# Performance work log

Hardware: AMD Instinct MI355X
Metric: run time of the kernel (lower is better)

## Reference

```python
import jax, jax.numpy as jnp
import numpy as np

B, T, I, H, L = 64, 512, 512, 512, 2

def _xavier(key, shape):
    fan_in, fan_out = shape
    limit = float(np.sqrt(6.0 / (fan_in + fan_out)))
    return jax.random.uniform(key, shape, jnp.float32, -limit, limit)

def setup_inputs() -> dict:
    key = jax.random.key(0)
    ks = jax.random.split(key, 16)
    x = jax.random.normal(ks[0], (B, T, I), jnp.float32)
    h = jax.random.normal(ks[1], (L, B, H), jnp.float32)
    c = jax.random.normal(ks[2], (L, B, H), jnp.float32)
    # Gate order: i, f, g, o (concatenated along output dim -> [*, 4H])
    W_x0 = jnp.concatenate([_xavier(ks[3 + j], (I, H)) for j in range(4)], axis=1)
    W_h0 = jnp.concatenate([_xavier(ks[7 + j], (H, H)) for j in range(4)], axis=1)
    W_x1 = jnp.concatenate([_xavier(ks[11], (H, H)), _xavier(ks[12], (H, H)),
                            _xavier(ks[13], (H, H)), _xavier(ks[14], (H, H))], axis=1)
    W_h1 = jnp.concatenate([jax.random.split(ks[15], 4)[j] is None or _xavier(jax.random.split(ks[15], 4)[j], (H, H)) for j in range(4)], axis=1)
    # 8 scalar biases per layer: (b_ii, b_hi, b_if, b_hf, b_ig, b_hg, b_io, b_ho); zero-init as in torch
    b0 = jnp.zeros((8,), jnp.float32)
    b1 = jnp.zeros((8,), jnp.float32)
    return {"x": x, "h": h, "c": c, "W_x0": W_x0, "W_h0": W_h0, "b0": b0,
            "W_x1": W_x1, "W_h1": W_h1, "b1": b1}

def _lstm_layer(xs, h0, c0, Wx, Wh, b):
    # xs: [B, T, D]; Wx: [D, 4H]; Wh: [H, 4H]; b: [8] scalars
    bg = b[0::2] + b[1::2]  # combined per-gate scalar biases [4]: i, f, g, o
    x_proj = jnp.einsum('btd,dk->btk', xs, Wx)  # precompute input GEMM: [B, T, 4H]

    def step(carry, xp_t):
        h, c = carry
        z = xp_t + h @ Wh  # [B, 4H]
        zi, zf, zg, zo = jnp.split(z, 4, axis=1)
        i = jax.nn.sigmoid(zi + bg[0])
        f = jax.nn.sigmoid(zf + bg[1])
        g = jnp.tanh(zg + bg[2])
        o = jax.nn.sigmoid(zo + bg[3])
        c_new = f * c + i * g
        h_new = o * jnp.tanh(c_new)
        return (h_new, c_new), h_new

    (hT, cT), ys = jax.lax.scan(step, (h0, c0), jnp.swapaxes(x_proj, 0, 1))
    return jnp.swapaxes(ys, 0, 1), hT, cT  # output [B, T, H]

def reference(x, h, c, W_x0, W_h0, b0, W_x1, W_h1, b1):
    out0, h0T, c0T = _lstm_layer(x, h[0], c[0], W_x0, W_h0, b0)
    out1, h1T, c1T = _lstm_layer(out0, h[1], c[1], W_x1, W_h1, b1)
    new_h = jnp.stack([h0T, h1T])  # [L, B, H]
    new_c = jnp.stack([c0T, c1T])
    return out1, new_h, new_c
```

## Files before the change

### kernel.cpp

```cpp
#include <hip/hip_runtime.h>
#include <hip/hip_bf16.h>

#define B_   64
#define T_   512
#define I_   512
#define H_   512
#define NBLK 128
#define NTHR 256

typedef short bf16x8 __attribute__((ext_vector_type(8)));
typedef float f32x4  __attribute__((ext_vector_type(4)));
typedef unsigned long long u64;
typedef unsigned short u16;

#define MFMA(a, b, c) __builtin_amdgcn_mfma_f32_16x16x32_bf16((a), (b), (c), 0, 0, 0)

__device__ __forceinline__ u16 f2b(float f) {
    __hip_bfloat16 h = __float2bfloat16(f);
    return __builtin_bit_cast(u16, h);
}

__device__ __forceinline__ u64 coh_ld64(const void* p) {
    return __hip_atomic_load((const u64*)p, __ATOMIC_RELAXED, __HIP_MEMORY_SCOPE_AGENT);
}
__device__ __forceinline__ void coh_st64(void* p, u64 v) {
    __hip_atomic_store((u64*)p, v, __ATOMIC_RELAXED, __HIP_MEMORY_SCOPE_AGENT);
}

__device__ __forceinline__ bool flag_ge(const int* f, int idx, int tgt) {
    return __hip_atomic_load(f + idx, __ATOMIC_RELAXED, __HIP_MEMORY_SCOPE_AGENT) >= tgt;
}

__global__ void k_init(const float* __restrict__ x, const float* __restrict__ h,
                       u16* __restrict__ xb, u16* __restrict__ h0ring, u16* __restrict__ h1ring,
                       int* __restrict__ flags0, int* __restrict__ flags1) {
    long i = (long)blockIdx.x * 256 + threadIdx.x;
    if (i < 2097152) {
        const float* p = x + i * 8;
        float4 a = *(const float4*)p;
        float4 b = *(const float4*)(p + 4);
        union { u16 s[8]; bf16x8 v; } u;
        u.s[0]=f2b(a.x); u.s[1]=f2b(a.y); u.s[2]=f2b(a.z); u.s[3]=f2b(a.w);
        u.s[4]=f2b(b.x); u.s[5]=f2b(b.y); u.s[6]=f2b(b.z); u.s[7]=f2b(b.w);
        *(bf16x8*)(xb + i * 8) = u.v;
    } else if (i < 2097152 + 8192) {
        long j = i - 2097152;
        const float* p = h + j * 8;
        #pragma unroll
        for (int jj = 0; jj < 8; ++jj) {
            long idx = j * 8 + jj;
            u16 v = f2b(p[jj]);
            if (idx < 32768) h0ring[7 * 32768 + idx] = v;
            else             h1ring[7 * 32768 + (idx - 32768)] = v;
        }
    } else if (i < 2097152 + 8192 + 512) {
        int j = (int)(i - (2097152 + 8192));
        if (j < 256) flags0[j] = 0; else flags1[j - 256] = 0;
    }
}

__global__ __launch_bounds__(NTHR, 1) void k_lstm(
    const u16* __restrict__ xb,
    const float* __restrict__ Wx0, const float* __restrict__ Wh0, const float* __restrict__ b0,
    const float* __restrict__ Wx1, const float* __restrict__ Wh1, const float* __restrict__ b1,
    const float* __restrict__ c_in,
    u16* __restrict__ h0ring, u16* __restrict__ h1ring,
    int* __restrict__ flags0, int* __restrict__ flags1,
    float* __restrict__ cs,
    float* __restrict__ out)
{
    const int tid  = threadIdx.x;
    const int bid  = blockIdx.x;
    const int lay  = bid >> 6;
    const int g    = (bid >> 4) & 3;
    const int u    = bid & 15;
    const int wave = tid >> 6;
    const int lane = tid & 63;
    const int n    = lane & 15;
    const int quad = lane >> 4;
    const int R0   = g * 16;
    const int U0   = u * 32;

    __shared__ __align__(16) u16   hstage[2][8192];
    __shared__ __align__(16) u16   sc_all[16 * 36];
    __shared__ __align__(16) float sc_h [4][16][8];

    const float* Wx = lay ? Wx1 : Wx0;
    const float* Wh = lay ? Wh1 : Wh0;
    const float* bb = lay ? b1  : b0;
    const float bi = bb[0] + bb[1];
    const float bf = bb[2] + bb[3];
    const float bg = bb[4] + bb[5];
    const float bo = bb[6] + bb[7];

    bf16x8 breg[2][32];
    #pragma unroll
    for (int ct = 0; ct < 2; ++ct) {
        const int gate = ct * 2 + (n >> 3);
        const int gcol = gate * 512 + U0 + wave * 8 + (n & 7);
        #pragma unroll
        for (int f = 0; f < 32; ++f) {
            const int kbase = f * 32 + quad * 8;
            bf16x8 w;
            #pragma unroll
            for (int j = 0; j < 8; ++j) {
                const int k = kbase + j;
                const float v = (k < 512) ? Wx[(size_t)k * 2048 + gcol]
                                          : Wh[(size_t)(k - 512) * 2048 + gcol];
                w[j] = (short)f2b(v);
            }
            breg[ct][f] = w;
        }
    }

    int* myflag = (lay ? flags1 : flags0) + g * 16 + u;
    const int fidx = g * 16 + n;
    (void)cs;

    float creg[4];
    if (n < 8) {
        #pragma unroll
        for (int r = 0; r < 4; ++r)
            creg[r] = c_in[(size_t)lay * 32768
                           + (size_t)(R0 + quad * 4 + r) * 512 + U0 + wave * 8 + n];
    }

    for (int t = 0; t < 512; ++t) {
        f32x4 acc0 = {0.f, 0.f, 0.f, 0.f};
        f32x4 acc1 = {0.f, 0.f, 0.f, 0.f};

        if (lay == 0) {
            const u16* px = xb + ((size_t)(R0 + n) * T_ + t) * I_;
            bf16x8 xa[16];
            #pragma unroll
            for (int f = 0; f < 16; ++f) xa[f] = *(const bf16x8*)(px + f * 32 + quad * 8);
            #pragma unroll
            for (int f = 0; f < 16; ++f) {
                acc0 = MFMA(xa[f], breg[0][f], acc0);
                acc1 = MFMA(xa[f], breg[1][f], acc1);
            }
            const bool bp = (t & 3) == 0;
            for (;;) {
                bool ok = flag_ge(flags0, fidx, t);
                if (bp) ok = ok && flag_ge(flags1, fidx, t - 4);
                if (__all(ok)) break;
                __builtin_amdgcn_s_sleep(1);
            }
            asm volatile("" ::: "memory");
            const u16* base = h0ring + (size_t)((t - 1) & 7) * 32768;
            u64 v[8];
            #pragma unroll
            for (int i = 0; i < 8; ++i) {
                const int s = i * 256 + tid;
                const int r = s >> 7, m = s & 127;
                v[i] = coh_ld64(base + (size_t)(R0 + r) * 512 + m * 4);
            }
            #pragma unroll
            for (int i = 0; i < 8; ++i) {
                const int s = i * 256 + tid;
                const int r = s >> 7, m = s & 127;
                const int uu = m >> 1, sub = m & 1;
                *(u64*)&hstage[0][r * 512 + (((uu ^ (r & 7)) << 3) | (sub << 2))] = v[i];
            }
            __syncthreads();
            #pragma unroll
            for (int f = 0; f < 16; ++f) {
                bf16x8 ha = *(const bf16x8*)
                    &hstage[0][n * 512 + (((f * 4 + quad) ^ (n & 7)) << 3)];
                acc0 = MFMA(ha, breg[0][16 + f], acc0);
                acc1 = MFMA(ha, breg[1][16 + f], acc1);
            }
        } else {
            for (;;) {
                bool ok = flag_ge(flags1, fidx, t) && flag_ge(flags0, fidx, t + 1);
                if (__all(ok)) break;
                __builtin_amdgcn_s_sleep(1);
            }
            asm volatile("" ::: "memory");
            const u16* base0 = h0ring + (size_t)(t & 7) * 32768;
            const u16* base1 = h1ring + (size_t)((t - 1) & 7) * 32768;
            u64 v0[8], v1[8];
            #pragma unroll
            for (int i = 0; i < 8; ++i) {
                const int s = i * 256 + tid;
                const int r = s >> 7, m = s & 127;
                v0[i] = coh_ld64(base0 + (size_t)(R0 + r) * 512 + m * 4);
                v1[i] = coh_ld64(base1 + (size_t)(R0 + r) * 512 + m * 4);
            }
            #pragma unroll
            for (int i = 0; i < 8; ++i) {
                const int s = i * 256 + tid;
                const int r = s >> 7, m = s & 127;
                const int uu = m >> 1, sub = m & 1;
                const int off = r * 512 + (((uu ^ (r & 7)) << 3) | (sub << 2));
                *(u64*)&hstage[0][off] = v0[i];
                *(u64*)&hstage[1][off] = v1[i];
            }
            __syncthreads();
            #pragma unroll
            for (int f = 0; f < 16; ++f) {
                const int off = n * 512 + (((f * 4 + quad) ^ (n & 7)) << 3);
                bf16x8 ha = *(const bf16x8*)&hstage[0][off];
                acc0 = MFMA(ha, breg[0][f], acc0);
                acc1 = MFMA(ha, breg[1][f], acc1);
                bf16x8 hb = *(const bf16x8*)&hstage[1][off];
                acc0 = MFMA(hb, breg[0][16 + f], acc0);
                acc1 = MFMA(hb, breg[1][16 + f], acc1);
            }
        }

        f32x4 x0, x1;
        #pragma unroll
        for (int r = 0; r < 4; ++r) {
            x0[r] = __shfl_xor(acc0[r], 8);
            x1[r] = __shfl_xor(acc1[r], 8);
        }
        if (n < 8) {
            #pragma unroll
            for (int r = 0; r < 4; ++r) {
                const int row = quad * 4 + r;
                const float zi = acc0[r] + bi;
                const float zf = x0[r]   + bf;
                const float zg = acc1[r] + bg;
                const float zo = x1[r]   + bo;
                const float ig = 1.f / (1.f + __expf(-zi));
                const float fg = 1.f / (1.f + __expf(-zf));
                const float gg = tanhf(zg);
                const float og = 1.f / (1.f + __expf(-zo));
                const float cn = fg * creg[r] + ig * gg;
                const float hn = og * tanhf(cn);
                creg[r] = cn;
                sc_all[row * 36 + wave * 8 + n] = f2b(hn);
                sc_h [wave][row][n] = hn;
            }
        }
        __syncthreads();

        if (wave == 0) {
            u16* ring = (lay ? h1ring : h0ring) + (size_t)(t & 7) * 32768;
            #pragma unroll
            for (int k = 0; k < 2; ++k) {
                const int j   = k * 64 + lane;
                const int row = j >> 3, s8 = j & 7;
                u64 vv = *(const u64*)&sc_all[row * 36 + s8 * 4];
                coh_st64(ring + (size_t)(R0 + row) * 512 + U0 + s8 * 4, vv);
            }
            asm volatile("s_waitcnt vmcnt(0)" ::: "memory");
            if (lane == 0)
                __hip_atomic_store(myflag, t + 1, __ATOMIC_RELAXED, __HIP_MEMORY_SCOPE_AGENT);
        }

        if (lay && lane < 16) {
            const float* s = &sc_h[wave][lane][0];
            f32x4 a  = *(const f32x4*)s;
            f32x4 b2 = *(const f32x4*)(s + 4);
            float* po = out + ((size_t)(R0 + lane) * T_ + t) * H_ + U0 + wave * 8;
            *(f32x4*)po       = a;
            *(f32x4*)(po + 4) = b2;
        }
        if (t == 511 && n < 8) {
            const size_t o1 = (size_t)B_ * T_ * H_;
            #pragma unroll
            for (int r = 0; r < 4; ++r) {
                const int grow = R0 + quad * 4 + r;
                out[o1 +         (size_t)lay * 32768 + (size_t)grow * 512 + U0 + wave * 8 + n]
                    = sc_h[wave][quad * 4 + r][n];
                out[o1 + 65536 + (size_t)lay * 32768 + (size_t)grow * 512 + U0 + wave * 8 + n]
                    = creg[r];
            }
        }
    }
}

extern "C" void kernel_launch(void* const* d_in, const int* in_sizes, int n_in,
                              void* d_out, int out_size, void* d_ws, size_t ws_size,
                              hipStream_t stream) {
    const float* x   = (const float*)d_in[0];
    const float* h   = (const float*)d_in[1];
    const float* c   = (const float*)d_in[2];
    const float* Wx0 = (const float*)d_in[3];
    const float* Wh0 = (const float*)d_in[4];
    const float* b0  = (const float*)d_in[5];
    const float* Wx1 = (const float*)d_in[6];
    const float* Wh1 = (const float*)d_in[7];
    const float* b1  = (const float*)d_in[8];
    float* out = (float*)d_out;

    u16* xb     = (u16*)d_ws;
    u16* h0ring = xb + 16777216;
    u16* h1ring = h0ring + 262144;
    int* flags0 = (int*)(h1ring + 262144);
    int* flags1 = flags0 + 256;
    float* cs   = (float*)(flags1 + 256);

    k_init<<<8226, 256, 0, stream>>>(x, h, xb, h0ring, h1ring, flags0, flags1);
    k_lstm<<<NBLK, NTHR, 0, stream>>>(xb, Wx0, Wh0, b0, Wx1, Wh1, b1, c,
                                      h0ring, h1ring, flags0, flags1, cs, out);
}
```

Baseline: 3.138 ms.

## Co-locate batch groups on one XCD and sync via L2-coherent sc0 accesses

Launches 256 blocks and keeps only half of them, then reads the hardware XCC id so each batch group's 32 blocks can check whether they share one XCD. If they do and an sc0 probe round-trip succeeds, the recurrent h ring and flags use sc0 global loads and stores that stay coherent within that XCD's L2, and h is read straight from global instead of being staged through LDS. Otherwise the kernel falls back to the original agent-scope atomic path. This aims to cut the per-step cross-XCD synchronisation latency, at the cost of depending on how the hardware schedules blocks onto XCDs, extra startup handshakes, and spin loops with no sleep.

Result: faster. 2.938 ms (-6.4%).

```diff
diff --git a/kernel.cpp b/kernel.cpp
--- a/kernel.cpp
+++ b/kernel.cpp
@@ -5,7 +5,6 @@
 #define T_   512
 #define I_   512
 #define H_   512
-#define NBLK 128
 #define NTHR 256
 
 typedef short bf16x8 __attribute__((ext_vector_type(8)));
@@ -26,14 +25,76 @@
 __device__ __forceinline__ void coh_st64(void* p, u64 v) {
     __hip_atomic_store((u64*)p, v, __ATOMIC_RELAXED, __HIP_MEMORY_SCOPE_AGENT);
 }
-
 __device__ __forceinline__ bool flag_ge(const int* f, int idx, int tgt) {
     return __hip_atomic_load(f + idx, __ATOMIC_RELAXED, __HIP_MEMORY_SCOPE_AGENT) >= tgt;
 }
 
-__global__ void k_init(const float* __restrict__ x, const float* __restrict__ h,
-                       u16* __restrict__ xb, u16* __restrict__ h0ring, u16* __restrict__ h1ring,
-                       int* __restrict__ flags0, int* __restrict__ flags1) {
+__device__ __forceinline__ int sc0_ld_i32(const int* p) {
+    int v;
+    asm volatile("global_load_dword %0, %1, off sc0\n\ts_waitcnt vmcnt(0)"
+                 : "=&v"(v) : "v"(p) : "memory");
+    return v;
+}
+__device__ __forceinline__ void sc0_st_i32(int* p, int v) {
+    asm volatile("global_store_dword %0, %1, off sc0" :: "v"(p), "v"(v) : "memory");
+}
+
+#define GLD16(O, A)                                                         \
+  asm volatile(                                                             \
+    "global_load_dwordx4 %0, %16, off sc0\n\t"                              \
+    "global_load_dwordx4 %1, %16, off offset:64 sc0\n\t"                    \
+    "global_load_dwordx4 %2, %16, off offset:128 sc0\n\t"                   \
+    "global_load_dwordx4 %3, %16, off offset:192 sc0\n\t"                   \
+    "global_load_dwordx4 %4, %16, off offset:256 sc0\n\t"                   \
+    "global_load_dwordx4 %5, %16, off offset:320 sc0\n\t"                   \
+    "global_load_dwordx4 %6, %16, off offset:384 sc0\n\t"                   \
+    "global_load_dwordx4 %7, %16, off offset:448 sc0\n\t"                   \
+    "global_load_dwordx4 %8, %16, off offset:512 sc0\n\t"                   \
+    "global_load_dwordx4 %9, %16, off offset:576 sc0\n\t"                   \
+    "global_load_dwordx4 %10, %16, off offset:640 sc0\n\t"                  \
+    "global_load_dwordx4 %11, %16, off offset:704 sc0\n\t"                  \
+    "global_load_dwordx4 %12, %16, off offset:768 sc0\n\t"                  \
+    "global_load_dwordx4 %13, %16, off offset:832 sc0\n\t"                  \
+    "global_load_dwordx4 %14, %16, off offset:896 sc0\n\t"                  \
+    "global_load_dwordx4 %15, %16, off offset:960 sc0\n\t"                  \
+    "s_waitcnt vmcnt(0)"                                                    \
+    : "=&v"(O[0]), "=&v"(O[1]), "=&v"(O[2]), "=&v"(O[3]),                   \
+      "=&v"(O[4]), "=&v"(O[5]), "=&v"(O[6]), "=&v"(O[7]),                   \
+      "=&v"(O[8]), "=&v"(O[9]), "=&v"(O[10]), "=&v"(O[11]),                 \
+      "=&v"(O[12]), "=&v"(O[13]), "=&v"(O[14]), "=&v"(O[15])                \
+    : "v"(A) : "memory")
+
+__device__ __forceinline__ void pub_local(u16* ring, int* fp, int fval,
+                                          const u16* sca, int lane, int U0) {
+    const int r0 = lane >> 3, s0 = lane & 7;
+    const int r1 = 8 + r0;
+    u64 q0 = *(const u64*)(sca + r0 * 36 + s0 * 4);
+    u64 q1 = *(const u64*)(sca + r1 * 36 + s0 * 4);
+    u16* d0 = ring + r0 * 512 + U0 + s0 * 4;
+    u16* d1 = ring + r1 * 512 + U0 + s0 * 4;
+    asm volatile(
+        "global_store_dwordx2 %0, %2, off sc0\n\t"
+        "global_store_dwordx2 %1, %3, off sc0\n\t"
+        "s_waitcnt vmcnt(0)"
+        :: "v"(d0), "v"(d1), "v"(q0), "v"(q1) : "memory");
+    if (lane == 0) sc0_st_i32(fp, fval);
+}
+
+__device__ __forceinline__ void pub_agent(u16* ring, int* fp, int fval,
+                                          const u16* sca, int lane, int R0, int U0) {
+    const int r0 = lane >> 3, s0 = lane & 7;
+    const int r1 = 8 + r0;
+    u64 q0 = *(const u64*)(sca + r0 * 36 + s0 * 4);
+    u64 q1 = *(const u64*)(sca + r1 * 36 + s0 * 4);
+    coh_st64(ring + (size_t)(R0 + r0) * 512 + U0 + s0 * 4, q0);
+    coh_st64(ring + (size_t)(R0 + r1) * 512 + U0 + s0 * 4, q1);
+    asm volatile("s_waitcnt vmcnt(0)" ::: "memory");
+    if (lane == 0)
+        __hip_atomic_store(fp, fval, __ATOMIC_RELAXED, __HIP_MEMORY_SCOPE_AGENT);
+}
+
+__global__ void k_init(const float* __restrict__ x, u16* __restrict__ xb,
+                       int* __restrict__ fl) {
     long i = (long)blockIdx.x * 256 + threadIdx.x;
     if (i < 2097152) {
         const float* p = x + i * 8;
@@ -43,19 +104,8 @@
         u.s[0]=f2b(a.x); u.s[1]=f2b(a.y); u.s[2]=f2b(a.z); u.s[3]=f2b(a.w);
         u.s[4]=f2b(b.x); u.s[5]=f2b(b.y); u.s[6]=f2b(b.z); u.s[7]=f2b(b.w);
         *(bf16x8*)(xb + i * 8) = u.v;
-    } else if (i < 2097152 + 8192) {
-        long j = i - 2097152;
-        const float* p = h + j * 8;
-        #pragma unroll
-        for (int jj = 0; jj < 8; ++jj) {
-            long idx = j * 8 + jj;
-            u16 v = f2b(p[jj]);
-            if (idx < 32768) h0ring[7 * 32768 + idx] = v;
-            else             h1ring[7 * 32768 + (idx - 32768)] = v;
-        }
-    } else if (i < 2097152 + 8192 + 512) {
-        int j = (int)(i - (2097152 + 8192));
-        if (j < 256) flags0[j] = 0; else flags1[j - 256] = 0;
+    } else if (i < 2097152 + 1024) {
+        fl[i - 2097152] = -1;
     }
 }
 
@@ -63,17 +113,21 @@
     const u16* __restrict__ xb,
     const float* __restrict__ Wx0, const float* __restrict__ Wh0, const float* __restrict__ b0,
     const float* __restrict__ Wx1, const float* __restrict__ Wh1, const float* __restrict__ b1,
-    const float* __restrict__ c_in,
-    u16* __restrict__ h0ring, u16* __restrict__ h1ring,
-    int* __restrict__ flags0, int* __restrict__ flags1,
-    float* __restrict__ cs,
+    const float* __restrict__ c_in, const float* __restrict__ h_in,
+    u16* __restrict__ h0ag, u16* __restrict__ h1ag,
+    u16* __restrict__ h0loc, u16* __restrict__ h1loc,
+    int* __restrict__ f0ag, int* __restrict__ f1ag,
+    int* __restrict__ f0loc, int* __restrict__ f1loc,
+    int* __restrict__ xcc_tab, int* __restrict__ probe, int* __restrict__ verd,
     float* __restrict__ out)
 {
+    const int bid = blockIdx.x;
+    if ((bid & 7) >= 4) return;
+    const int g   = bid & 7;
+    const int jj  = bid >> 3;
+    const int lay = jj >> 4;
+    const int u   = jj & 15;
     const int tid  = threadIdx.x;
-    const int bid  = blockIdx.x;
-    const int lay  = bid >> 6;
-    const int g    = (bid >> 4) & 3;
-    const int u    = bid & 15;
     const int wave = tid >> 6;
     const int lane = tid & 63;
     const int n    = lane & 15;
@@ -84,6 +138,13 @@
     __shared__ __align__(16) u16   hstage[2][8192];
     __shared__ __align__(16) u16   sc_all[16 * 36];
     __shared__ __align__(16) float sc_h [4][16][8];
+    __shared__ int s_local;
+    __shared__ int s_ver;
+
+    int myxcc;
+    asm volatile("s_getreg_b32 %0, hwreg(HW_REG_XCC_ID)" : "=s"(myxcc));
+    if (tid == 0)
+        __hip_atomic_store(xcc_tab + bid, myxcc, __ATOMIC_RELAXED, __HIP_MEMORY_SCOPE_AGENT);
 
     const float* Wx = lay ? Wx1 : Wx0;
     const float* Wh = lay ? Wh1 : Wh0;
@@ -113,10 +174,6 @@
         }
     }
 
-    int* myflag = (lay ? flags1 : flags0) + g * 16 + u;
-    const int fidx = g * 16 + n;
-    (void)cs;
-
     float creg[4];
     if (n < 8) {
         #pragma unroll
@@ -125,10 +182,220 @@
                            + (size_t)(R0 + quad * 4 + r) * 512 + U0 + wave * 8 + n];
     }
 
+    if (wave == 0) {
+        const int member = (lane & 31) * 8 + g;
+        int v;
+        for (;;) {
+            v = __hip_atomic_load(xcc_tab + member, __ATOMIC_RELAXED, __HIP_MEMORY_SCOPE_AGENT);
+            if (__all(v != -1)) break;
+            __builtin_amdgcn_s_sleep(8);
+        }
+        const int v0 = __shfl(v, 0);
+        if (lane == 0) s_local = __all(v == v0) ? 1 : 0;
+    }
+    __syncthreads();
+
+    int myver = 0;
+    if (s_local) {
+        if (tid == 0) sc0_st_i32(probe + bid, 0x5a5a0000 | bid);
+        if (wave == 0) {
+            const int member = (lane & 31) * 8 + g;
+            const int want = 0x5a5a0000 | member;
+            int ok = 0;
+            for (int it = 0; it < 4000 && !ok; ++it)
+                ok = __all(sc0_ld_i32(probe + member) == want) ? 1 : 0;
+            if (lane == 0) s_ver = ok;
+        }
+        __syncthreads();
+        myver = s_ver;
+    }
+
+    if (tid == 0)
+        __hip_atomic_store(verd + bid, myver, __ATOMIC_RELAXED, __HIP_MEMORY_SCOPE_AGENT);
+    if (wave == 0) {
+        const int member = (lane & 31) * 8 + g;
+        int v;
+        for (;;) {
+            v = __hip_atomic_load(verd + member, __ATOMIC_RELAXED, __HIP_MEMORY_SCOPE_AGENT);
+            if (__all(v != -1)) break;
+            __builtin_amdgcn_s_sleep(8);
+        }
+        if (lane == 0) s_local = __all(v == 1) ? 1 : 0;
+    }
+    __syncthreads();
+    const bool loc = (s_local != 0);
+
+    if (n < 8) {
+        #pragma unroll
+        for (int r = 0; r < 4; ++r) {
+            const int row = quad * 4 + r;
+            const float hv = h_in[(size_t)lay * 32768
+                                  + (size_t)(R0 + row) * 512 + U0 + wave * 8 + n];
+            sc_all[row * 36 + wave * 8 + n] = f2b(hv);
+        }
+    }
+    __syncthreads();
+    if (loc) {
+        if (wave == 3)
+            pub_local((lay ? h1loc : h0loc) + (size_t)g * 65536 + 7 * 8192,
+                      (lay ? f1loc : f0loc) + g * 16 + u, 0, sc_all, lane, U0);
+    } else {
+        if (wave == 0)
+            pub_agent((lay ? h1ag : h0ag) + (size_t)7 * 32768,
+                      (lay ? f1ag : f0ag) + g * 16 + u, 0, sc_all, lane, R0, U0);
+    }
+
+    const int fidx = g * 16 + n;
+
+    if (loc) {
+        int* pp0 = f0loc + g * 16 + n;
+        int* pp1 = f1loc + g * 16 + n;
+        if (lay == 0) {
+            for (int t = 0; t < 512; ++t) {
+                f32x4 acc0 = {0.f,0.f,0.f,0.f}, acc1 = {0.f,0.f,0.f,0.f};
+                const u16* px = xb + ((size_t)(R0 + n) * T_ + t) * I_;
+                bf16x8 xa[16];
+                #pragma unroll
+                for (int f = 0; f < 16; ++f) xa[f] = *(const bf16x8*)(px + f * 32 + quad * 8);
+                #pragma unroll
+                for (int f = 0; f < 16; ++f) {
+                    acc0 = MFMA(xa[f], breg[0][f], acc0);
+                    acc1 = MFMA(xa[f], breg[1][f], acc1);
+                }
+                if ((t & 3) == 0) {
+                    for (;;) {
+                        int a_ = sc0_ld_i32(pp0);
+                        int b_ = sc0_ld_i32(pp1);
+                        if (__all(a_ >= t && b_ >= t - 4)) break;
+                    }
+                } else {
+                    while (!__all(sc0_ld_i32(pp0) >= t)) {}
+                }
+                const u16* ha = h0loc + (size_t)g * 65536
+                                + (size_t)((t - 1) & 7) * 8192 + n * 512 + quad * 8;
+                bf16x8 hf[16];
+                GLD16(hf, ha);
+                #pragma unroll
+                for (int f = 0; f < 16; ++f) {
+                    acc0 = MFMA(hf[f], breg[0][16 + f], acc0);
+                    acc1 = MFMA(hf[f], breg[1][16 + f], acc1);
+                }
+                f32x4 x0, x1;
+                #pragma unroll
+                for (int r = 0; r < 4; ++r) {
+                    x0[r] = __shfl_xor(acc0[r], 8);
+                    x1[r] = __shfl_xor(acc1[r], 8);
+                }
+                if (n < 8) {
+                    #pragma unroll
+                    for (int r = 0; r < 4; ++r) {
+                        const int row = quad * 4 + r;
+                        const float zi = acc0[r] + bi, zf = x0[r] + bf;
+                        const float zg = acc1[r] + bg, zo = x1[r] + bo;
+                        const float ig = 1.f / (1.f + __expf(-zi));
+                        const float fg = 1.f / (1.f + __expf(-zf));
+                        const float gg = tanhf(zg);
+                        const float og = 1.f / (1.f + __expf(-zo));
+                        const float cn = fg * creg[r] + ig * gg;
+                        const float hn = og * tanhf(cn);
+                        creg[r] = cn;
+                        sc_all[row * 36 + wave * 8 + n] = f2b(hn);
+                        sc_h[wave][row][n] = hn;
+                    }
+                }
+                __syncthreads();
+                if (wave == (t & 3))
+                    pub_local(h0loc + (size_t)g * 65536 + (size_t)(t & 7) * 8192,
+                              f0loc + g * 16 + u, t + 1, sc_all, lane, U0);
+                if (t == 511 && n < 8) {
+                    const size_t o1 = (size_t)B_ * T_ * H_;
+                    #pragma unroll
+                    for (int r = 0; r < 4; ++r) {
+                        const int grow = R0 + quad * 4 + r;
+                        out[o1 + (size_t)grow * 512 + U0 + wave * 8 + n]
+                            = sc_h[wave][quad * 4 + r][n];
+                        out[o1 + 65536 + (size_t)grow * 512 + U0 + wave * 8 + n] = creg[r];
+                    }
+                }
+            }
+        } else {
+            for (int t = 0; t < 512; ++t) {
+                for (;;) {
+                    int a_ = sc0_ld_i32(pp1);
+                    int b_ = sc0_ld_i32(pp0);
+                    if (__all(a_ >= t && b_ >= t + 1)) break;
+                }
+                const u16* a0p = h0loc + (size_t)g * 65536
+                                 + (size_t)(t & 7) * 8192 + n * 512 + quad * 8;
+                const u16* a1p = h1loc + (size_t)g * 65536
+                                 + (size_t)((t - 1) & 7) * 8192 + n * 512 + quad * 8;
+                f32x4 acc0 = {0.f,0.f,0.f,0.f}, acc1 = {0.f,0.f,0.f,0.f};
+                bf16x8 hf[16];
+                GLD16(hf, a0p);
+                #pragma unroll
+                for (int f = 0; f < 16; ++f) {
+                    acc0 = MFMA(hf[f], breg[0][f], acc0);
+                    acc1 = MFMA(hf[f], breg[1][f], acc1);
+                }
+                GLD16(hf, a1p);
+                #pragma unroll
+                for (int f = 0; f < 16; ++f) {
+                    acc0 = MFMA(hf[f], breg[0][16 + f], acc0);
+                    acc1 = MFMA(hf[f], breg[1][16 + f], acc1);
+                }
+                f32x4 x0, x1;
+                #pragma unroll
+                for (int r = 0; r < 4; ++r) {
+                    x0[r] = __shfl_xor(acc0[r], 8);
+                    x1[r] = __shfl_xor(acc1[r], 8);
+                }
+                if (n < 8) {
+                    #pragma unroll
+                    for (int r = 0; r < 4; ++r) {
+                        const int row = quad * 4 + r;
+                        const float zi = acc0[r] + bi, zf = x0[r] + bf;
+                        const float zg = acc1[r] + bg, zo = x1[r] + bo;
+                        const float ig = 1.f / (1.f + __expf(-zi));
+                        const float fg = 1.f / (1.f + __expf(-zf));
+                        const float gg = tanhf(zg);
+                        const float og = 1.f / (1.f + __expf(-zo));
+                        const float cn = fg * creg[r] + ig * gg;
+                        const float hn = og * tanhf(cn);
+                        creg[r] = cn;
+                        sc_all[row * 36 + wave * 8 + n] = f2b(hn);
+                        sc_h[wave][row][n] = hn;
+                    }
+                }
+                __syncthreads();
+                if (wave == (t & 3))
+                    pub_local(h1loc + (size_t)g * 65536 + (size_t)(t & 7) * 8192,
+                              f1loc + g * 16 + u, t + 1, sc_all, lane, U0);
+                if (lane < 16) {
+                    const float* s = &sc_h[wave][lane][0];
+                    f32x4 a  = *(const f32x4*)s;
+                    f32x4 b2 = *(const f32x4*)(s + 4);
+                    float* po = out + ((size_t)(R0 + lane) * T_ + t) * H_ + U0 + wave * 8;
+                    *(f32x4*)po       = a;
+                    *(f32x4*)(po + 4) = b2;
+                }
+                if (t == 511 && n < 8) {
+                    const size_t o1 = (size_t)B_ * T_ * H_;
+                    #pragma unroll
+                    for (int r = 0; r < 4; ++r) {
+                        const int grow = R0 + quad * 4 + r;
+                        out[o1 + 32768 + (size_t)grow * 512 + U0 + wave * 8 + n]
+                            = sc_h[wave][quad * 4 + r][n];
+                        out[o1 + 65536 + 32768 + (size_t)grow * 512 + U0 + wave * 8 + n]
+                            = creg[r];
+                    }
+                }
+            }
+        }
+        return;
+    }
+
     for (int t = 0; t < 512; ++t) {
-        f32x4 acc0 = {0.f, 0.f, 0.f, 0.f};
-        f32x4 acc1 = {0.f, 0.f, 0.f, 0.f};
-
+        f32x4 acc0 = {0.f,0.f,0.f,0.f}, acc1 = {0.f,0.f,0.f,0.f};
         if (lay == 0) {
             const u16* px = xb + ((size_t)(R0 + n) * T_ + t) * I_;
             bf16x8 xa[16];
@@ -141,13 +408,13 @@
             }
             const bool bp = (t & 3) == 0;
             for (;;) {
-                bool ok = flag_ge(flags0, fidx, t);
-                if (bp) ok = ok && flag_ge(flags1, fidx, t - 4);
+                bool ok = flag_ge(f0ag, fidx, t);
+                if (bp) ok = ok && flag_ge(f1ag, fidx, t - 4);
                 if (__all(ok)) break;
                 __builtin_amdgcn_s_sleep(1);
             }
             asm volatile("" ::: "memory");
-            const u16* base = h0ring + (size_t)((t - 1) & 7) * 32768;
+            const u16* base = h0ag + (size_t)((t - 1) & 7) * 32768;
             u64 v[8];
             #pragma unroll
             for (int i = 0; i < 8; ++i) {
@@ -172,13 +439,13 @@
             }
         } else {
             for (;;) {
-                bool ok = flag_ge(flags1, fidx, t) && flag_ge(flags0, fidx, t + 1);
+                bool ok = flag_ge(f1ag, fidx, t) && flag_ge(f0ag, fidx, t + 1);
                 if (__all(ok)) break;
                 __builtin_amdgcn_s_sleep(1);
             }
             asm volatile("" ::: "memory");
-            const u16* base0 = h0ring + (size_t)(t & 7) * 32768;
-            const u16* base1 = h1ring + (size_t)((t - 1) & 7) * 32768;
+            const u16* base0 = h0ag + (size_t)(t & 7) * 32768;
+            const u16* base1 = h1ag + (size_t)((t - 1) & 7) * 32768;
             u64 v0[8], v1[8];
             #pragma unroll
             for (int i = 0; i < 8; ++i) {
@@ -208,7 +475,6 @@
                 acc1 = MFMA(hb, breg[1][16 + f], acc1);
             }
         }
-
         f32x4 x0, x1;
         #pragma unroll
         for (int r = 0; r < 4; ++r) {
@@ -219,10 +485,8 @@
             #pragma unroll
             for (int r = 0; r < 4; ++r) {
                 const int row = quad * 4 + r;
-                const float zi = acc0[r] + bi;
-                const float zf = x0[r]   + bf;
-                const float zg = acc1[r] + bg;
-                const float zo = x1[r]   + bo;
+                const float zi = acc0[r] + bi, zf = x0[r] + bf;
+                const float zg = acc1[r] + bg, zo = x1[r] + bo;
                 const float ig = 1.f / (1.f + __expf(-zi));
                 const float fg = 1.f / (1.f + __expf(-zf));
                 const float gg = tanhf(zg);
@@ -231,25 +495,13 @@
                 const float hn = og * tanhf(cn);
                 creg[r] = cn;
                 sc_all[row * 36 + wave * 8 + n] = f2b(hn);
-                sc_h [wave][row][n] = hn;
+                sc_h[wave][row][n] = hn;
             }
         }
         __syncthreads();
-
-        if (wave == 0) {
-            u16* ring = (lay ? h1ring : h0ring) + (size_t)(t & 7) * 32768;
-            #pragma unroll
-            for (int k = 0; k < 2; ++k) {
-                const int j   = k * 64 + lane;
-                const int row = j >> 3, s8 = j & 7;
-                u64 vv = *(const u64*)&sc_all[row * 36 + s8 * 4];
-                coh_st64(ring + (size_t)(R0 + row) * 512 + U0 + s8 * 4, vv);
-            }
-            asm volatile("s_waitcnt vmcnt(0)" ::: "memory");
-            if (lane == 0)
-                __hip_atomic_store(myflag, t + 1, __ATOMIC_RELAXED, __HIP_MEMORY_SCOPE_AGENT);
-        }
-
+        if (wave == 0)
+            pub_agent((lay ? h1ag : h0ag) + (size_t)(t & 7) * 32768,
+                      (lay ? f1ag : f0ag) + g * 16 + u, t + 1, sc_all, lane, R0, U0);
         if (lay && lane < 16) {
             const float* s = &sc_h[wave][lane][0];
             f32x4 a  = *(const f32x4*)s;
@@ -263,7 +515,7 @@
             #pragma unroll
             for (int r = 0; r < 4; ++r) {
                 const int grow = R0 + quad * 4 + r;
-                out[o1 +         (size_t)lay * 32768 + (size_t)grow * 512 + U0 + wave * 8 + n]
+                out[o1 + (size_t)lay * 32768 + (size_t)grow * 512 + U0 + wave * 8 + n]
                     = sc_h[wave][quad * 4 + r][n];
                 out[o1 + 65536 + (size_t)lay * 32768 + (size_t)grow * 512 + U0 + wave * 8 + n]
                     = creg[r];
@@ -287,13 +539,20 @@
     float* out = (float*)d_out;
 
     u16* xb     = (u16*)d_ws;
-    u16* h0ring = xb + 16777216;
-    u16* h1ring = h0ring + 262144;
-    int* flags0 = (int*)(h1ring + 262144);
-    int* flags1 = flags0 + 256;
-    float* cs   = (float*)(flags1 + 256);
-
-    k_init<<<8226, 256, 0, stream>>>(x, h, xb, h0ring, h1ring, flags0, flags1);
-    k_lstm<<<NBLK, NTHR, 0, stream>>>(xb, Wx0, Wh0, b0, Wx1, Wh1, b1, c,
-                                      h0ring, h1ring, flags0, flags1, cs, out);
-}
+    u16* h0ag   = xb + 16777216;
+    u16* h1ag   = h0ag + 262144;
+    u16* h0loc  = h1ag + 262144;
+    u16* h1loc  = h0loc + 262144;
+    int* f0ag   = (int*)(h1loc + 262144);
+    int* f1ag   = f0ag + 64;
+    int* f0loc  = f1ag + 64;
+    int* f1loc  = f0loc + 64;
+    int* xcc    = f1loc + 64;
+    int* probe  = xcc + 256;
+    int* verd   = probe + 256;
+
+    k_init<<<8196, 256, 0, stream>>>(x, xb, f0ag);
+    k_lstm<<<256, NTHR, 0, stream>>>(xb, Wx0, Wh0, b0, Wx1, Wh1, b1, c, h,
+                                     h0ag, h1ag, h0loc, h1loc,
+                                     f0ag, f1ag, f0loc, f1loc, xcc, probe, verd, out);
+}
```
